# Kernel optimization log

Hardware: AMD Instinct MI355X
Metric: run time of the kernel (lower is better)

## Reference

```python
import jax, jax.numpy as jnp
import numpy as np

EMBED = 1024
HEADS = 16
INTERNAL = 1024  # embedding_dim // downsample_rate
HEAD_DIM = INTERNAL // HEADS


def setup_inputs() -> dict:
    key = jax.random.key(0)
    ks = jax.random.split(key, 12)
    B, S = 2, 2048
    s_in = 1.0 / np.sqrt(EMBED)
    s_out = 1.0 / np.sqrt(INTERNAL)
    return {
        "queries": jax.random.normal(ks[0], (B, S, EMBED), jnp.float32),
        "keys": jax.random.normal(ks[1], (B, S, EMBED), jnp.float32),
        "values": jax.random.normal(ks[2], (B, S, EMBED), jnp.float32),
        "Wq": jax.random.uniform(ks[3], (EMBED, INTERNAL), jnp.float32, -s_in, s_in),
        "bq": jax.random.uniform(ks[4], (INTERNAL,), jnp.float32, -s_in, s_in),
        "Wk": jax.random.uniform(ks[5], (EMBED, INTERNAL), jnp.float32, -s_in, s_in),
        "bk": jax.random.uniform(ks[6], (INTERNAL,), jnp.float32, -s_in, s_in),
        "Wv": jax.random.uniform(ks[7], (EMBED, INTERNAL), jnp.float32, -s_in, s_in),
        "bv": jax.random.uniform(ks[8], (INTERNAL,), jnp.float32, -s_in, s_in),
        "Wo": jax.random.uniform(ks[9], (INTERNAL, EMBED), jnp.float32, -s_out, s_out),
        "bo": jax.random.uniform(ks[10], (EMBED,), jnp.float32, -s_out, s_out),
    }


def _split_heads(x):
    B, S, D = x.shape
    return x.reshape(B, S, HEADS, D // HEADS).transpose(0, 2, 1, 3)  # bhsd


def reference(queries, keys, values, Wq, bq, Wk, bk, Wv, bv, Wo, bo):
    q = _split_heads(queries @ Wq + bq)
    k = _split_heads(keys @ Wk + bk)
    v = _split_heads(values @ Wv + bv)
    # NOTE: original scales by 1/sqrt(internal_dim), not 1/sqrt(head_dim)
    scale = 1.0 / np.sqrt(INTERNAL).astype(np.float32)
    scores = jnp.einsum("bhqd,bhkd->bhqk", q, k) * scale
    probs = jax.nn.softmax(scores, axis=-1)
    out = jnp.einsum("bhqk,bhkd->bhqd", probs, v)
    B, H, S, Dh = out.shape
    out = out.transpose(0, 2, 1, 3).reshape(B, S, H * Dh)
    return out @ Wo + bo
```

## Files before the change

### kernel.cpp

```cpp
#include <hip/hip_runtime.h>
#include <stdint.h>

typedef unsigned short u16;
typedef __attribute__((ext_vector_type(8))) short short8;
typedef __attribute__((ext_vector_type(4))) float f32x4;
typedef __attribute__((ext_vector_type(16))) float f32x16;
typedef __attribute__((ext_vector_type(8))) unsigned short u16x8;
typedef __attribute__((ext_vector_type(4))) unsigned short u16x4;
typedef __attribute__((ext_vector_type(4))) uint32_t u32x4;

#if __has_builtin(__builtin_amdgcn_exp2f)
#define EXP2(x) __builtin_amdgcn_exp2f(x)
#else
#define EXP2(x) exp2f(x)
#endif

__device__ __forceinline__ u16 f2bf(float f) {
  union { float f; uint32_t u; } v; v.f = f;
  uint32_t r = (v.u + 0x7FFFu + ((v.u >> 16) & 1u)) >> 16;
  return (u16)r;
}

__device__ __forceinline__ float bf2f(u16 u) {
  union { uint32_t u; float f; } v; v.u = ((uint32_t)u) << 16;
  return v.f;
}

__device__ __forceinline__ uint32_t pack2(float a, float b) {
  return (__float_as_uint(b) & 0xffff0000u) | (__float_as_uint(a) >> 16);
}

__device__ __forceinline__ void gload_lds16(const void* g, void* l) {
  __builtin_amdgcn_global_load_lds(
      (const __attribute__((address_space(1))) void*)g,
      (__attribute__((address_space(3))) void*)l,
      16, 0, 0);
}

__global__ __launch_bounds__(256) void cvt_x(const float* __restrict__ q,
                                             const float* __restrict__ k,
                                             const float* __restrict__ v,
                                             u16* __restrict__ dst) {
  const float* src = blockIdx.z == 0 ? q : (blockIdx.z == 1 ? k : v);
  u16* d = dst + (size_t)blockIdx.z * (4096u * 1024u);
  size_t i = ((size_t)blockIdx.x * 256 + threadIdx.x) * 8;
  float4 a = *(const float4*)(src + i);
  float4 b = *(const float4*)(src + i + 4);
  u16x8 o;
  o[0] = f2bf(a.x); o[1] = f2bf(a.y); o[2] = f2bf(a.z); o[3] = f2bf(a.w);
  o[4] = f2bf(b.x); o[5] = f2bf(b.y); o[6] = f2bf(b.z); o[7] = f2bf(b.w);
  *(u16x8*)(d + i) = o;
}

__global__ __launch_bounds__(256) void cvt_wt(const float* __restrict__ Wq,
                                              const float* __restrict__ Wk,
                                              const float* __restrict__ Wv,
                                              const float* __restrict__ Wo,
                                              u16* __restrict__ Wt4) {
  const float* W = blockIdx.z == 0 ? Wq : (blockIdx.z == 1 ? Wk
                   : (blockIdx.z == 2 ? Wv : Wo));
  u16* Wt = Wt4 + (size_t)blockIdx.z * (1024u * 1024u);
  __shared__ u16 tile[64][65];
  int kt = blockIdx.x * 64, nt = blockIdx.y * 64;
  int t = threadIdx.x;
#pragma unroll
  for (int r = 0; r < 4; ++r) {
    int id = t + r * 256;
    int kk = id >> 4, c4 = id & 15;
    float4 vv = *(const float4*)(W + (size_t)(kt + kk) * 1024 + nt + c4 * 4);
    tile[kk][c4 * 4 + 0] = f2bf(vv.x);
    tile[kk][c4 * 4 + 1] = f2bf(vv.y);
    tile[kk][c4 * 4 + 2] = f2bf(vv.z);
    tile[kk][c4 * 4 + 3] = f2bf(vv.w);
  }
  __syncthreads();
#pragma unroll
  for (int r = 0; r < 4; ++r) {
    int id = t + r * 256;
    int n = id >> 4, kc = id & 15;
    u16x4 o;
    o[0] = tile[kc * 4 + 0][n];
    o[1] = tile[kc * 4 + 1][n];
    o[2] = tile[kc * 4 + 2][n];
    o[3] = tile[kc * 4 + 3][n];
    *(u16x4*)(Wt + (size_t)(nt + n) * 1024 + kt + kc * 4) = o;
  }
}

template <bool F32OUT>
__device__ __forceinline__ void gemm_tile(const u16* __restrict__ A,
                                          const u16* __restrict__ Bt,
                                          const float* __restrict__ bias,
                                          u16* __restrict__ Cb,
                                          float* __restrict__ Cf,
                                          float scale, int bm, int bn) {
  __shared__ u16 Alds[128 * 64];
  __shared__ u16 Blds[128 * 64];
  const int tid = threadIdx.x;
  const int lane = tid & 63, w = tid >> 6;
  const int wm = (w >> 1) * 64, wn = (w & 1) * 64;
  const int l15 = lane & 15, lg = lane >> 4;

  f32x4 acc[4][4] = {};

  int srow[4], scol[4], soff[4];
#pragma unroll
  for (int i = 0; i < 4; ++i) {
    int o = (w * 4 + i) * 1024 + lane * 16;
    int row = o >> 7;
    int kc = ((o >> 4) & 7) ^ (row & 7);
    srow[i] = row; scol[i] = kc * 8; soff[i] = o;
  }

  for (int kt = 0; kt < 16; ++kt) {
    __syncthreads();
#pragma unroll
    for (int i = 0; i < 4; ++i) {
      gload_lds16(A + (size_t)(bm * 128 + srow[i]) * 1024 + kt * 64 + scol[i],
                  (char*)Alds + soff[i]);
      gload_lds16(Bt + (size_t)(bn * 128 + srow[i]) * 1024 + kt * 64 + scol[i],
                  (char*)Blds + soff[i]);
    }
    __syncthreads();
#pragma unroll
    for (int ks = 0; ks < 2; ++ks) {
      short8 af[4], bf[4];
#pragma unroll
      for (int m = 0; m < 4; ++m) {
        int r = wm + m * 16 + l15;
        int byt = r * 128 + ((ks * 64 + lg * 16) ^ ((r & 7) << 4));
        af[m] = *(const short8*)((const char*)Alds + byt);
      }
#pragma unroll
      for (int n = 0; n < 4; ++n) {
        int r = wn + n * 16 + l15;
        int byt = r * 128 + ((ks * 64 + lg * 16) ^ ((r & 7) << 4));
        bf[n] = *(const short8*)((const char*)Blds + byt);
      }
#pragma unroll
      for (int m = 0; m < 4; ++m)
#pragma unroll
        for (int n = 0; n < 4; ++n)
          acc[m][n] = __builtin_amdgcn_mfma_f32_16x16x32_bf16(
              af[m], bf[n], acc[m][n], 0, 0, 0);
    }
  }
#pragma unroll
  for (int m = 0; m < 4; ++m) {
    int row0 = bm * 128 + wm + m * 16 + lg * 4;
#pragma unroll
    for (int n = 0; n < 4; ++n) {
      int col = bn * 128 + wn + n * 16 + l15;
      float bvv = bias[col];
#pragma unroll
      for (int r = 0; r < 4; ++r) {
        float v = (acc[m][n][r] + bvv) * scale;
        if (F32OUT)
          Cf[(size_t)(row0 + r) * 1024 + col] = v;
        else
          Cb[(size_t)(row0 + r) * 1024 + col] = f2bf(v);
      }
    }
  }
}

__global__ __launch_bounds__(256) void proj_kernel(const u16* __restrict__ X3,
                                                   const u16* __restrict__ Wt3,
                                                   const float* __restrict__ bq,
                                                   const float* __restrict__ bk,
                                                   const float* __restrict__ bv,
                                                   u16* __restrict__ out3) {
  int z = blockIdx.z;
  const float* bias = z == 0 ? bq : (z == 1 ? bk : bv);
  float scale = z == 0 ? 0.045084220f : 1.0f;
  gemm_tile<false>(X3 + (size_t)z * 4096 * 1024, Wt3 + (size_t)z * 1024 * 1024,
                   bias, out3 + (size_t)z * 4096 * 1024, nullptr, scale,
                   blockIdx.x, blockIdx.y);
}

__global__ __launch_bounds__(256) void outproj_kernel(const u16* __restrict__ Att,
                                                      const u16* __restrict__ Wot,
                                                      const float* __restrict__ bo,
                                                      float* __restrict__ out) {
  gemm_tile<true>(Att, Wot, bo, nullptr, out, 1.0f, blockIdx.x, blockIdx.y);
}

__global__ __launch_bounds__(256) void vt_kernel(const u16* __restrict__ v,
                                                 u16* __restrict__ vt) {
  int bh = blockIdx.y;
  int sbase = blockIdx.x * 64;
  int b = bh >> 4, h = bh & 15;
  __shared__ u16 tile[64][65];
  int t = threadIdx.x;
#pragma unroll
  for (int r = 0; r < 2; ++r) {
    int id = t + r * 256;
    int s = id >> 3, dc = id & 7;
    u16x8 x = *(const u16x8*)(v + (size_t)(b * 2048 + sbase + s) * 1024 +
                              h * 64 + dc * 8);
#pragma unroll
    for (int j = 0; j < 8; ++j) tile[s][dc * 8 + j] = x[j];
  }
  __syncthreads();
#pragma unroll
  for (int r = 0; r < 2; ++r) {
    int id = t + r * 256;
    int d = id >> 3, sc = id & 7;
    u16x8 o;
#pragma unroll
    for (int j = 0; j < 8; ++j) o[j] = tile[sc * 8 + j][d];
    *(u16x8*)(vt + ((size_t)bh * 64 + d) * 2048 + sbase + sc * 8) = o;
  }
}

__global__ __launch_bounds__(256, 2) void attn_kernel(const u16* __restrict__ q,
                                                      const u16* __restrict__ k,
                                                      const u16* __restrict__ vt,
                                                      u16* __restrict__ attp,
                                                      float* __restrict__ lp) {
  __shared__ u16 smem[16384];
  const int tid = threadIdx.x, lane = tid & 63, w = tid >> 6;
  const int l31 = lane & 31, hi = lane >> 5;
  const int bh = blockIdx.y, b = bh >> 4, h = bh & 15;
  const int z = blockIdx.z;
  const int qb = blockIdx.x * 256 + w * 64;

  short8 qf[2][4];
#pragma unroll
  for (int g = 0; g < 2; ++g) {
    const u16* qrow =
        q + (size_t)(b * 2048 + qb + g * 32 + l31) * 1024 + h * 64 + hi * 8;
#pragma unroll
    for (int s = 0; s < 4; ++s) qf[g][s] = *(const short8*)(qrow + s * 16);
  }

  f32x16 acc[2][2] = {};
  float lsum[2] = {0.f, 0.f};

  int scol[2], rowK[2], rowV[2];
#pragma unroll
  for (int i = 0; i < 2; ++i) {
    int gi = i * 256 + tid;
    int row = gi & 63, c16 = gi >> 6;
    scol[i] = c16 * 8;
    rowV[i] = row;
    rowK[i] = row ^ ((((row >> 2) ^ (row >> 3)) & 1) ? 12 : 0);
  }
  const u16* ksrc = k + (size_t)b * 2048 * 1024 + h * 64;
  const u16* vsrc = vt + (size_t)bh * 64 * 2048;
  const int kb0 = z * 1024;

#pragma unroll
  for (int i = 0; i < 2; ++i) {
    gload_lds16(ksrc + (size_t)(kb0 + rowK[i]) * 1024 + scol[i],
                (char*)smem + i * 4096 + tid * 16);
    gload_lds16(vsrc + (size_t)rowV[i] * 2048 + kb0 + scol[i],
                (char*)smem + 8192 + i * 4096 + tid * 16);
  }

  for (int tt = 0; tt < 16; ++tt) {
    const int cur = tt & 1;
    __syncthreads();
    if (tt + 1 < 16) {
      char* dst = (char*)smem + (cur ^ 1) * 16384;
      const int kb2 = kb0 + (tt + 1) * 64;
#pragma unroll
      for (int i = 0; i < 2; ++i) {
        gload_lds16(ksrc + (size_t)(kb2 + rowK[i]) * 1024 + scol[i],
                    dst + i * 4096 + tid * 16);
        gload_lds16(vsrc + (size_t)rowV[i] * 2048 + kb2 + scol[i],
                    dst + 8192 + i * 4096 + tid * 16);
      }
    }
    const char* KL = (const char*)smem + cur * 16384;
    const char* VL = KL + 8192;

#pragma unroll
    for (int kg = 0; kg < 2; ++kg) {
      short8 ak[4], bv[4];
#pragma unroll
      for (int s = 0; s < 4; ++s)
        ak[s] = *(const short8*)(KL + (s * 2 + hi) * 1024 +
                                 (kg * 32 + l31) * 16);
#pragma unroll
      for (int c = 0; c < 2; ++c)
#pragma unroll
        for (int half = 0; half < 2; ++half)
          bv[c * 2 + half] =
              *(const short8*)(VL + (kg * 4 + c * 2 + hi) * 1024 +
                               (half * 32 + l31) * 16);
#pragma unroll
      for (int g = 0; g < 2; ++g) {
        f32x16 sc = {};
#pragma unroll
        for (int s = 0; s < 4; ++s)
          sc = __builtin_amdgcn_mfma_f32_32x32x16_bf16(ak[s], qf[g][s], sc,
                                                       0, 0, 0);
        float p[16];
#pragma unroll
        for (int e = 0; e < 16; ++e) p[e] = EXP2(sc[e]);
#pragma unroll
        for (int e = 0; e < 16; e += 4)
          lsum[g] += (p[e] + p[e + 1]) + (p[e + 2] + p[e + 3]);
#pragma unroll
        for (int c = 0; c < 2; ++c) {
          u32x4 fw;
          fw[0] = pack2(p[8 * c + 0], p[8 * c + 1]);
          fw[1] = pack2(p[8 * c + 2], p[8 * c + 3]);
          fw[2] = pack2(p[8 * c + 4], p[8 * c + 5]);
          fw[3] = pack2(p[8 * c + 6], p[8 * c + 7]);
          short8 pf = __builtin_bit_cast(short8, fw);
          acc[g][0] = __builtin_amdgcn_mfma_f32_32x32x16_bf16(
              pf, bv[c * 2 + 0], acc[g][0], 0, 0, 0);
          acc[g][1] = __builtin_amdgcn_mfma_f32_32x32x16_bf16(
              pf, bv[c * 2 + 1], acc[g][1], 0, 0, 0);
        }
      }
    }
  }

  float lt[2];
#pragma unroll
  for (int g = 0; g < 2; ++g) lt[g] = lsum[g] + __shfl_xor(lsum[g], 32);
  if (hi == 0) {
    float* lbase = lp + (size_t)z * 65536;
#pragma unroll
    for (int g = 0; g < 2; ++g)
      lbase[(size_t)(b * 2048 + qb + g * 32 + l31) * 16 + h] = lt[g];
  }

  __syncthreads();
  u16* tw = smem + w * 4096;
#pragma unroll
  for (int g = 0; g < 2; ++g)
#pragma unroll
    for (int r = 0; r < 16; ++r) {
      int rq = (r & 3) + 8 * (r >> 2) + 4 * hi;
      int row = g * 32 + rq;
      tw[row * 64 + l31] = f2bf(acc[g][0][r]);
      tw[row * 64 + 32 + l31] = f2bf(acc[g][1][r]);
    }
  asm volatile("s_waitcnt lgkmcnt(0)" ::: "memory");
  __builtin_amdgcn_sched_barrier(0);
  u16* abase = attp + (size_t)z * (4096u * 1024u) +
               (size_t)(b * 2048 + qb) * 1024 + h * 64;
#pragma unroll
  for (int i = 0; i < 8; ++i) {
    int id = lane + i * 64;
    int row = id >> 3, ch = id & 7;
    u16x8 vv = *(const u16x8*)(tw + row * 64 + ch * 8);
    *(u16x8*)(abase + (size_t)row * 1024 + ch * 8) = vv;
  }
}

__global__ __launch_bounds__(256) void merge_kernel(const u16* __restrict__ a0,
                                                    const u16* __restrict__ a1,
                                                    const float* __restrict__ lp,
                                                    u16* __restrict__ out) {
  size_t i0 = ((size_t)blockIdx.x * 256 + threadIdx.x) * 8;
  int row = (int)(i0 >> 10);
  int head = (int)((i0 >> 6) & 15);
  float l = lp[(size_t)row * 16 + head] + lp[65536 + (size_t)row * 16 + head];
  float rinv = 1.0f / l;
  u16x8 x0 = *(const u16x8*)(a0 + i0);
  u16x8 x1 = *(const u16x8*)(a1 + i0);
  u16x8 o;
#pragma unroll
  for (int j = 0; j < 8; ++j)
    o[j] = f2bf((bf2f(x0[j]) + bf2f(x1[j])) * rinv);
  *(u16x8*)(out + i0) = o;
}

extern "C" void kernel_launch(void* const* d_in, const int* in_sizes, int n_in,
                              void* d_out, int out_size, void* d_ws,
                              size_t ws_size, hipStream_t stream) {
  const float* Q  = (const float*)d_in[0];
  const float* K  = (const float*)d_in[1];
  const float* V  = (const float*)d_in[2];
  const float* Wq = (const float*)d_in[3];
  const float* bq = (const float*)d_in[4];
  const float* Wk = (const float*)d_in[5];
  const float* bk = (const float*)d_in[6];
  const float* Wv = (const float*)d_in[7];
  const float* bv = (const float*)d_in[8];
  const float* Wo = (const float*)d_in[9];
  const float* bo = (const float*)d_in[10];
  float* out = (float*)d_out;

  u16* ws = (u16*)d_ws;
  const size_t SZX = (size_t)4096 * 1024;
  const size_t SZW = (size_t)1024 * 1024;
  u16* Xbf   = ws;
  u16* Wtbf  = ws + 3 * SZX;
  u16* QKVbf = Wtbf + 4 * SZW;
  u16* VTbf  = QKVbf + 3 * SZX;
  u16* ATTbf = VTbf + SZX;
  u16*   attP  = Xbf;
  float* lsumP = (float*)(Xbf + 2 * SZX);

  hipLaunchKernelGGL(cvt_x, dim3(2048, 1, 3), dim3(256), 0, stream, Q, K, V,
                     Xbf);
  hipLaunchKernelGGL(cvt_wt, dim3(16, 16, 4), dim3(256), 0, stream, Wq, Wk, Wv,
                     Wo, Wtbf);
  hipLaunchKernelGGL(proj_kernel, dim3(32, 8, 3), dim3(256), 0, stream, Xbf,
                     Wtbf, bq, bk, bv, QKVbf);
  hipLaunchKernelGGL(vt_kernel, dim3(32, 32), dim3(256), 0, stream,
                     QKVbf + 2 * SZX, VTbf);
  hipLaunchKernelGGL(attn_kernel, dim3(8, 32, 2), dim3(256), 0, stream, QKVbf,
                     QKVbf + SZX, VTbf, attP, lsumP);
  hipLaunchKernelGGL(merge_kernel, dim3(2048), dim3(256), 0, stream, attP,
                     attP + SZX, lsumP, ATTbf);
  hipLaunchKernelGGL(outproj_kernel, dim3(32, 8), dim3(256), 0, stream, ATTbf,
                     Wtbf + 3 * SZW, bo, out);
}
```

Measured before the change: 123.4 us.

## Split attention keys four ways, add XCD-aware block swizzle to GEMMs and attention

```diff
diff --git a/kernel.cpp b/kernel.cpp
--- a/kernel.cpp
+++ b/kernel.cpp
@@ -35,6 +35,12 @@
       (const __attribute__((address_space(1))) void*)g,
       (__attribute__((address_space(3))) void*)l,
       16, 0, 0);
+}
+
+__device__ __forceinline__ int xcd_swz() {
+  int flat = blockIdx.x + gridDim.x * (blockIdx.y + gridDim.y * blockIdx.z);
+  int nwg = gridDim.x * gridDim.y * gridDim.z;
+  return (flat & 7) * (nwg >> 3) + (flat >> 3);
 }
 
 __global__ __launch_bounds__(256) void cvt_x(const float* __restrict__ q,
@@ -170,19 +176,22 @@
                                                    const float* __restrict__ bk,
                                                    const float* __restrict__ bv,
                                                    u16* __restrict__ out3) {
-  int z = blockIdx.z;
+  int l = xcd_swz();
+  int bm = l & 31, bn = (l >> 5) & 7, z = l >> 8;
   const float* bias = z == 0 ? bq : (z == 1 ? bk : bv);
   float scale = z == 0 ? 0.045084220f : 1.0f;
   gemm_tile<false>(X3 + (size_t)z * 4096 * 1024, Wt3 + (size_t)z * 1024 * 1024,
                    bias, out3 + (size_t)z * 4096 * 1024, nullptr, scale,
-                   blockIdx.x, blockIdx.y);
+                   bm, bn);
 }
 
 __global__ __launch_bounds__(256) void outproj_kernel(const u16* __restrict__ Att,
                                                       const u16* __restrict__ Wot,
                                                       const float* __restrict__ bo,
                                                       float* __restrict__ out) {
-  gemm_tile<true>(Att, Wot, bo, nullptr, out, 1.0f, blockIdx.x, blockIdx.y);
+  int l = xcd_swz();
+  int bm = l & 31, bn = l >> 5;
+  gemm_tile<true>(Att, Wot, bo, nullptr, out, 1.0f, bm, bn);
 }
 
 __global__ __launch_bounds__(256) void vt_kernel(const u16* __restrict__ v,
@@ -213,17 +222,19 @@
   }
 }
 
-__global__ __launch_bounds__(256, 2) void attn_kernel(const u16* __restrict__ q,
+__global__ __launch_bounds__(256, 4) void attn_kernel(const u16* __restrict__ q,
                                                       const u16* __restrict__ k,
                                                       const u16* __restrict__ vt,
-                                                      u16* __restrict__ attp,
+                                                      u16* __restrict__ attp0,
+                                                      u16* __restrict__ attp3,
                                                       float* __restrict__ lp) {
   __shared__ u16 smem[16384];
   const int tid = threadIdx.x, lane = tid & 63, w = tid >> 6;
   const int l31 = lane & 31, hi = lane >> 5;
-  const int bh = blockIdx.y, b = bh >> 4, h = bh & 15;
-  const int z = blockIdx.z;
-  const int qb = blockIdx.x * 256 + w * 64;
+  int l = xcd_swz();
+  const int bx = l & 7, bh = (l >> 3) & 31, z = l >> 8;
+  const int b = bh >> 4, h = bh & 15;
+  const int qb = bx * 256 + w * 64;
 
   short8 qf[2][4];
 #pragma unroll
@@ -248,7 +259,7 @@
   }
   const u16* ksrc = k + (size_t)b * 2048 * 1024 + h * 64;
   const u16* vsrc = vt + (size_t)bh * 64 * 2048;
-  const int kb0 = z * 1024;
+  const int kb0 = z * 512;
 
 #pragma unroll
   for (int i = 0; i < 2; ++i) {
@@ -258,10 +269,10 @@
                 (char*)smem + 8192 + i * 4096 + tid * 16);
   }
 
-  for (int tt = 0; tt < 16; ++tt) {
+  for (int tt = 0; tt < 8; ++tt) {
     const int cur = tt & 1;
     __syncthreads();
-    if (tt + 1 < 16) {
+    if (tt + 1 < 8) {
       char* dst = (char*)smem + (cur ^ 1) * 16384;
       const int kb2 = kb0 + (tt + 1) * 64;
 #pragma unroll
@@ -342,8 +353,8 @@
     }
   asm volatile("s_waitcnt lgkmcnt(0)" ::: "memory");
   __builtin_amdgcn_sched_barrier(0);
-  u16* abase = attp + (size_t)z * (4096u * 1024u) +
-               (size_t)(b * 2048 + qb) * 1024 + h * 64;
+  u16* pbase = (z == 3) ? attp3 : (attp0 + (size_t)z * (4096u * 1024u));
+  u16* abase = pbase + (size_t)(b * 2048 + qb) * 1024 + h * 64;
 #pragma unroll
   for (int i = 0; i < 8; ++i) {
     int id = lane + i * 64;
@@ -353,21 +364,26 @@
   }
 }
 
-__global__ __launch_bounds__(256) void merge_kernel(const u16* __restrict__ a0,
-                                                    const u16* __restrict__ a1,
+__global__ __launch_bounds__(256) void merge_kernel(const u16* __restrict__ p012,
+                                                    const u16* __restrict__ p3,
                                                     const float* __restrict__ lp,
                                                     u16* __restrict__ out) {
+  const size_t SZX = (size_t)4096 * 1024;
   size_t i0 = ((size_t)blockIdx.x * 256 + threadIdx.x) * 8;
   int row = (int)(i0 >> 10);
   int head = (int)((i0 >> 6) & 15);
-  float l = lp[(size_t)row * 16 + head] + lp[65536 + (size_t)row * 16 + head];
-  float rinv = 1.0f / l;
-  u16x8 x0 = *(const u16x8*)(a0 + i0);
-  u16x8 x1 = *(const u16x8*)(a1 + i0);
+  size_t li = (size_t)row * 16 + head;
+  float lsm = (lp[li] + lp[65536 + li]) + (lp[2 * 65536 + li] + lp[3 * 65536 + li]);
+  float rinv = 1.0f / lsm;
+  u16x8 x0 = *(const u16x8*)(p012 + i0);
+  u16x8 x1 = *(const u16x8*)(p012 + SZX + i0);
+  u16x8 x2 = *(const u16x8*)(p012 + 2 * SZX + i0);
+  u16x8 x3 = *(const u16x8*)(p3 + i0);
   u16x8 o;
 #pragma unroll
   for (int j = 0; j < 8; ++j)
-    o[j] = f2bf((bf2f(x0[j]) + bf2f(x1[j])) * rinv);
+    o[j] = f2bf(((bf2f(x0[j]) + bf2f(x1[j])) + (bf2f(x2[j]) + bf2f(x3[j]))) *
+                rinv);
   *(u16x8*)(out + i0) = o;
 }
 
@@ -395,8 +411,9 @@
   u16* QKVbf = Wtbf + 4 * SZW;
   u16* VTbf  = QKVbf + 3 * SZX;
   u16* ATTbf = VTbf + SZX;
-  u16*   attP  = Xbf;
-  float* lsumP = (float*)(Xbf + 2 * SZX);
+  u16*   attP012 = Xbf;
+  u16*   attP3   = (u16*)d_out;
+  float* lsumP   = out + 2 * 1024 * 1024;
 
   hipLaunchKernelGGL(cvt_x, dim3(2048, 1, 3), dim3(256), 0, stream, Q, K, V,
                      Xbf);
@@ -406,10 +423,10 @@
                      Wtbf, bq, bk, bv, QKVbf);
   hipLaunchKernelGGL(vt_kernel, dim3(32, 32), dim3(256), 0, stream,
                      QKVbf + 2 * SZX, VTbf);
-  hipLaunchKernelGGL(attn_kernel, dim3(8, 32, 2), dim3(256), 0, stream, QKVbf,
-                     QKVbf + SZX, VTbf, attP, lsumP);
-  hipLaunchKernelGGL(merge_kernel, dim3(2048), dim3(256), 0, stream, attP,
-                     attP + SZX, lsumP, ATTbf);
+  hipLaunchKernelGGL(attn_kernel, dim3(8, 32, 4), dim3(256), 0, stream, QKVbf,
+                     QKVbf + SZX, VTbf, attP012, attP3, lsumP);
+  hipLaunchKernelGGL(merge_kernel, dim3(2048), dim3(256), 0, stream, attP012,
+                     attP3, lsumP, ATTbf);
   hipLaunchKernelGGL(outproj_kernel, dim3(32, 8), dim3(256), 0, stream, ATTbf,
                      Wtbf + 3 * SZW, bo, out);
 }
```

Measured after the change: 411.5 us. +233.5%, slower.
